# Optimization experiments

Hardware: AMD Instinct MI355X
Metric: run time of the kernel (lower is better)

The kernel has to match this reference:

```python
import jax, jax.numpy as jnp
import numpy as np

B, C, T, V = 8, 64, 16, 207
H, WSZ = 8, 4
EPS = 1e-5


def setup_inputs() -> dict:
    key = jax.random.key(0)
    ks = jax.random.split(key, 16)
    def w(k, shape):
        return jax.random.normal(k, shape, jnp.float32) * 0.02
    inp = {"x": jax.random.normal(ks[0], (B, C, T, V), jnp.float32)}
    for i, s in enumerate("ab"):
        o = 1 + i * 4
        inp[f"qkv_w_{s}"] = w(ks[o], (C, 3 * C))
        inp[f"qkv_b_{s}"] = jnp.zeros((3 * C,), jnp.float32)
        inp[f"proj_w_{s}"] = w(ks[o + 1], (C, C))
        inp[f"proj_b_{s}"] = jnp.zeros((C,), jnp.float32)
        inp[f"ffn_w1_{s}"] = w(ks[o + 2], (C, 4 * C))
        inp[f"ffn_b1_{s}"] = jnp.zeros((4 * C,), jnp.float32)
        inp[f"ffn_w2_{s}"] = w(ks[o + 3], (4 * C, C))
        inp[f"ffn_b2_{s}"] = jnp.zeros((C,), jnp.float32)
        inp[f"ln_{s}1_g"] = jnp.ones((C, T, V), jnp.float32)
        inp[f"ln_{s}1_b"] = jnp.zeros((C, T, V), jnp.float32)
        inp[f"ln_{s}2_g"] = jnp.ones((C, T, V), jnp.float32)
        inp[f"ln_{s}2_b"] = jnp.zeros((C, T, V), jnp.float32)
    inp["n_head"] = H
    inp["window_size"] = WSZ
    return inp


def _layer_norm(x, g, b):
    # LayerNorm over (C, T, V) dims of [B, C, T, V]
    mu = jnp.mean(x, axis=(1, 2, 3), keepdims=True)
    var = jnp.var(x, axis=(1, 2, 3), keepdims=True)
    return (x - mu) / jnp.sqrt(var + EPS) * g + b


def _window_att(x, wqkv, bqkv, wo, bo, n_head, wsz):
    # Joint spatio-temporal attention within windows of `wsz` timesteps.
    b_, c_, t_, v_ = x.shape
    nw = t_ // wsz
    dh = c_ // n_head
    # [B,C,T,V] -> [B,T,V,C] -> [B,nW, wsz*V, C]
    xt = jnp.transpose(x, (0, 2, 3, 1)).reshape(b_, nw, wsz * v_, c_)
    qkv = xt @ wqkv + bqkv  # [B,nW,N,3C]
    q, k, v = jnp.split(qkv, 3, axis=-1)
    def heads(t):
        return t.reshape(b_, nw, -1, n_head, dh).transpose(0, 1, 3, 2, 4)  # [B,nW,H,N,dh]
    q, k, v = heads(q), heads(k), heads(v)
    scale = 1.0 / jnp.sqrt(jnp.asarray(dh, jnp.float32))
    att = jax.nn.softmax(jnp.einsum('bwhnd,bwhmd->bwhnm', q, k) * scale, axis=-1)
    out = jnp.einsum('bwhnm,bwhmd->bwhnd', att, v)
    out = out.transpose(0, 1, 3, 2, 4).reshape(b_, nw, wsz * v_, c_) @ wo + bo
    return out.reshape(b_, t_, v_, c_).transpose(0, 3, 1, 2)


def _ffn(x, w1, b1, w2, b2):
    h = jax.nn.relu(jnp.einsum('bctv,cd->bdtv', x, w1) + b1[None, :, None, None])
    return jnp.einsum('bdtv,dc->bctv', h, w2) + b2[None, :, None, None]


def _block(x, wqkv, bqkv, wo, bo, w1, b1, w2, b2, g1, be1, g2, be2, n_head, wsz):
    x = _window_att(x, wqkv, bqkv, wo, bo, n_head, wsz) + x
    x = _layer_norm(x, g1, be1)
    x = _ffn(x, w1, b1, w2, b2) + x
    x = _layer_norm(x, g2, be2)
    # cyclic shift along time by shift_pixel = wsz // 2
    return jnp.roll(x, -(wsz // 2), axis=2)


def reference(x, qkv_w_a, qkv_b_a, proj_w_a, proj_b_a, ffn_w1_a, ffn_b1_a, ffn_w2_a, ffn_b2_a,
              ln_a1_g, ln_a1_b, ln_a2_g, ln_a2_b,
              qkv_w_b, qkv_b_b, proj_w_b, proj_b_b, ffn_w1_b, ffn_b1_b, ffn_w2_b, ffn_b2_b,
              ln_b1_g, ln_b1_b, ln_b2_g, ln_b2_b, n_head, window_size):
    x = _block(x, qkv_w_a, qkv_b_a, proj_w_a, proj_b_a, ffn_w1_a, ffn_b1_a, ffn_w2_a, ffn_b2_a,
               ln_a1_g, ln_a1_b, ln_a2_g, ln_a2_b, n_head, window_size)
    x = _block(x, qkv_w_b, qkv_b_b, proj_w_b, proj_b_b, ffn_w1_b, ffn_b1_b, ffn_w2_b, ffn_b2_b,
               ln_b1_g, ln_b1_b, ln_b2_g, ln_b2_b, n_head, window_size)
    return x
```

## Files before the change

kernel.cpp:

```cpp
#include <hip/hip_runtime.h>
#include <hip/hip_bf16.h>

#define Bb  8
#define Cc  64
#define Tt  16
#define Vv  207
#define Hh  8
#define DH  8
#define NW  4
#define WSZ 4
#define Nn  (WSZ*Vv)
#define NP  832
#define TV  (Tt*Vv)
#define CTV (Cc*Tt*Vv)
#define S   (Bb*CTV)
#define NBWH (Bb*NW*Hh)
#define EPSF 1e-5f
#define QSCALE 0.51006971401146f

typedef __attribute__((ext_vector_type(4))) short bf16x4;
typedef __attribute__((ext_vector_type(4))) float f32x4;
typedef __attribute__((ext_vector_type(2))) unsigned int u32x2;

static __device__ __forceinline__ short f2bf(float f) {
    union { float f; unsigned u; } v; v.f = f;
    unsigned r = (v.u + 0x7FFFu + ((v.u >> 16) & 1u)) >> 16;
    return (short)r;
}

static __device__ __forceinline__ bf16x4 pack4(float a, float b, float c, float d) {
    unsigned ua = __builtin_bit_cast(unsigned, a) + 0x8000u;
    unsigned ub = __builtin_bit_cast(unsigned, b) + 0x8000u;
    unsigned uc = __builtin_bit_cast(unsigned, c) + 0x8000u;
    unsigned ud = __builtin_bit_cast(unsigned, d) + 0x8000u;
    u32x2 t;
    t[0] = (ua >> 16) | (ub & 0xFFFF0000u);
    t[1] = (uc >> 16) | (ud & 0xFFFF0000u);
    return __builtin_bit_cast(bf16x4, t);
}

__global__ void prep_kernel(short* __restrict__ qb, short* __restrict__ kb,
                            short* __restrict__ vtb, float* __restrict__ stats) {
    int i = blockIdx.x*256 + threadIdx.x;
    if (i < 64) stats[i] = 0.f;
    if (i < NBWH*NP*8) {
        int bwh = i / (NP*8); int rest = i % (NP*8);
        int n = rest >> 3; int d = 8 + (rest & 7);
        kb[((size_t)bwh*NP + n)*16 + d] = 0;
        int d2 = 8 + rest / NP; int n2 = rest % NP;
        vtb[((size_t)bwh*16 + d2)*NP + n2] = (d2 == 8) ? (short)0x3F80 : (short)0;
    }
    if (i < NBWH*32) {
        int bwh = i >> 5; int rest = i & 31;
        int n = Nn + (rest >> 3); int d = rest & 7;
        qb[((size_t)bwh*NP + n)*8 + d] = 0;
        kb[((size_t)bwh*NP + n)*16 + d] = 0;
        int d3 = rest >> 2; int n3 = Nn + (rest & 3);
        vtb[((size_t)bwh*16 + d3)*NP + n3] = 0;
    }
}

__global__ __launch_bounds__(256) void qkv_kernel(const float* __restrict__ xin,
        const float* __restrict__ w, const float* __restrict__ bias,
        short* __restrict__ qb, short* __restrict__ kb, short* __restrict__ vtb) {
    __shared__ short wqs[3072*4];
    __shared__ float bqs[192];
    int tid = threadIdx.x;
    int b = blockIdx.x / 52;
    int r0 = (blockIdx.x % 52) * 64;
    const float* xb = xin + (size_t)b*CTV;
    for (int s = tid; s < 3072; s += 256) {
        int nt = s >> 8; int kc = (s >> 6) & 3; int ln = s & 63;
        int li = ln & 15; int q = ln >> 4;
        bf16x4 f;
        #pragma unroll
        for (int j = 0; j < 4; ++j)
            f[j] = f2bf(w[(kc*16 + q*4 + j)*192 + nt*16 + li]);
        *((bf16x4*)&wqs[s*4]) = f;
    }
    if (tid < 192) bqs[tid] = bias[tid];
    __syncthreads();

    int lane = tid & 63; int wv = tid >> 6;
    int l15 = lane & 15; int quad = lane >> 4;
    int r = r0 + wv*16 + l15;
    bool valid = r < TV;
    int rc = valid ? r : TV-1;
    bf16x4 xf[4];
    #pragma unroll
    for (int kc = 0; kc < 4; ++kc) {
        #pragma unroll
        for (int j = 0; j < 4; ++j)
            xf[kc][j] = f2bf(xb[(size_t)(kc*16 + quad*4 + j)*TV + rc]);
    }
    int t = rc / Vv; int vv = rc % Vv;
    int w_ = t >> 2; int tw = t & 3;
    int n = tw*Vv + vv;
    int bwbase = (b*NW + w_)*Hh;

    #pragma unroll
    for (int nt = 0; nt < 12; ++nt) {
        float4 bb = *((const float4*)&bqs[nt*16 + quad*4]);
        f32x4 acc = {bb.x, bb.y, bb.z, bb.w};
        #pragma unroll
        for (int kc = 0; kc < 4; ++kc) {
            bf16x4 wf = *((const bf16x4*)&wqs[((nt*4 + kc)*64 + lane)*4]);
            acc = __builtin_amdgcn_mfma_f32_16x16x16bf16_1k(wf, xf[kc], acc, 0, 0, 0);
        }
        if (valid) {
            int which = nt >> 2;
            #pragma unroll
            for (int j = 0; j < 4; ++j) {
                int cc = (nt & 3)*16 + quad*4 + j;
                int h = cc >> 3; int d = cc & 7;
                int bwh = bwbase + h;
                if (which == 0)      qb[((size_t)bwh*NP + n)*8 + d] = f2bf(acc[j]*QSCALE);
                else if (which == 1) kb[((size_t)bwh*NP + n)*16 + d] = f2bf(acc[j]);
                else                 vtb[((size_t)bwh*16 + d)*NP + n] = f2bf(acc[j]);
            }
        }
    }
}

__global__ __launch_bounds__(1024) void attn_kernel(const short* __restrict__ qb,
        const short* __restrict__ kb, const short* __restrict__ vtb,
        short* __restrict__ att) {
    __shared__ short ks[NP*20];
    __shared__ short vs[10*840];
    int bwh = blockIdx.x;
    int tid = threadIdx.x;
    int lane = tid & 63;
    int wv = tid >> 6;
    int quad = lane >> 4;
    int l15 = lane & 15;

    const u32x2* kg = (const u32x2*)(kb + (size_t)bwh*NP*16);
    for (int idx = tid; idx < NP*4; idx += 1024) {
        int n = idx >> 2; int j = idx & 3;
        *((u32x2*)&ks[n*20 + j*4]) = kg[idx];
    }
    const u32x2* vg = (const u32x2*)(vtb + (size_t)bwh*16*NP);
    for (int idx = tid; idx < 9*208; idx += 1024) {
        int rr = idx / 208; int j = idx % 208;
        *((u32x2*)&vs[rr*840 + j*4]) = vg[rr*208 + j];
    }
    if (tid < 210) *((u32x2*)&vs[9*840 + tid*4]) = (u32x2){0u, 0u};
    __syncthreads();

    int nm = (wv < 4) ? 4 : 3;
    const short* qbase = qb + (size_t)bwh*NP*8;
    bf16x4 aq[4];
    f32x4 oacc[4];
    #pragma unroll
    for (int i = 0; i < 4; ++i) {
        aq[i] = (bf16x4){0,0,0,0};
        oacc[i] = (f32x4){0.f,0.f,0.f,0.f};
        if (i < nm && quad < 2)
            aq[i] = *(const bf16x4*)(qbase + (((wv + 16*i)*16 + l15)*8 + quad*4));
    }
    const short* kls = &ks[l15*20 + quad*4];
    const short* vls = &vs[((l15 < 9) ? l15 : 9)*840 + quad*4];

    for (int nt = 0; nt < 52; ++nt) {
        bf16x4 ak = *(const bf16x4*)(kls + nt*320);
        bf16x4 av = *(const bf16x4*)(vls + nt*16);
        bool mask = (nt == 51) && (quad == 3);
        #pragma unroll
        for (int i = 0; i < 4; ++i) {
            if (i < nm) {
                f32x4 s = __builtin_amdgcn_mfma_f32_16x16x16bf16_1k(
                              ak, aq[i], (f32x4){0.f,0.f,0.f,0.f}, 0, 0, 0);
                bf16x4 pb = pack4(__builtin_amdgcn_exp2f(s[0]), __builtin_amdgcn_exp2f(s[1]),
                                  __builtin_amdgcn_exp2f(s[2]), __builtin_amdgcn_exp2f(s[3]));
                if (mask) pb = (bf16x4){0,0,0,0};
                oacc[i] = __builtin_amdgcn_mfma_f32_16x16x16bf16_1k(av, pb, oacc[i], 0, 0, 0);
            }
        }
    }
    int h = bwh & 7; int bw = bwh >> 3;
    #pragma unroll
    for (int i = 0; i < 4; ++i) {
        if (i < nm) {
            float ls = __shfl(oacc[i][0], 32 + l15, 64);
            float inv = 1.f / ls;
            int m = (wv + 16*i)*16 + l15;
            if (quad < 2 && m < Nn) {
                bf16x4 ov = pack4(oacc[i][0]*inv, oacc[i][1]*inv,
                                  oacc[i][2]*inv, oacc[i][3]*inv);
                *((bf16x4*)&att[((size_t)bw*Nn + m)*Cc + h*DH + quad*4]) = ov;
            }
        }
    }
}

__global__ __launch_bounds__(256) void proj_kernel(const short* __restrict__ att,
        const float* __restrict__ wo, const float* __restrict__ bo,
        const float* __restrict__ resid, float* __restrict__ out,
        float* __restrict__ stats) {
    __shared__ short wos[1024*4];
    __shared__ float bos[64];
    __shared__ float r1[256], r2[256];
    int tid = threadIdx.x;
    int b = blockIdx.x / 52;
    int r0 = (blockIdx.x % 52) * 64;
    const float* xb = resid + (size_t)b*CTV;
    for (int s = tid; s < 1024; s += 256) {
        int nt = s >> 8; int kc = (s >> 6) & 3; int ln = s & 63;
        int li = ln & 15; int q = ln >> 4;
        bf16x4 f;
        #pragma unroll
        for (int j = 0; j < 4; ++j)
            f[j] = f2bf(wo[(kc*16 + q*4 + j)*64 + nt*16 + li]);
        *((bf16x4*)&wos[s*4]) = f;
    }
    if (tid < 64) bos[tid] = bo[tid];
    __syncthreads();

    int lane = tid & 63; int wv = tid >> 6;
    int l15 = lane & 15; int quad = lane >> 4;
    int r = r0 + wv*16 + l15;
    bool valid = r < TV;
    int rc = valid ? r : TV-1;
    int t = rc / Vv; int vv = rc % Vv;
    int w_ = t >> 2; int tw = t & 3;
    int n = tw*Vv + vv;
    int bw = b*NW + w_;
    const short* arow = att + ((size_t)bw*Nn + n)*Cc;
    bf16x4 af[4];
    #pragma unroll
    for (int kc = 0; kc < 4; ++kc)
        af[kc] = *((const bf16x4*)&arow[kc*16 + quad*4]);

    f32x4 acc[4];
    #pragma unroll
    for (int nt = 0; nt < 4; ++nt) {
        float4 bb = *((const float4*)&bos[nt*16 + quad*4]);
        acc[nt] = (f32x4){bb.x, bb.y, bb.z, bb.w};
        #pragma unroll
        for (int kc = 0; kc < 4; ++kc) {
            bf16x4 wf = *((const bf16x4*)&wos[((nt*4 + kc)*64 + lane)*4]);
            acc[nt] = __builtin_amdgcn_mfma_f32_16x16x16bf16_1k(wf, af[kc], acc[nt], 0, 0, 0);
        }
    }
    float s1 = 0.f, s2 = 0.f;
    if (valid) {
        #pragma unroll
        for (int nt = 0; nt < 4; ++nt) {
            #pragma unroll
            for (int j = 0; j < 4; ++j) {
                int c_out = nt*16 + quad*4 + j;
                size_t oi = (size_t)b*CTV + (size_t)c_out*TV + r;
                float val = acc[nt][j] + xb[(size_t)c_out*TV + r];
                out[oi] = val;
                s1 += val; s2 += val*val;
            }
        }
    }
    r1[tid] = s1; r2[tid] = s2;
    __syncthreads();
    for (int o = 128; o > 0; o >>= 1) {
        if (tid < o) { r1[tid] += r1[tid+o]; r2[tid] += r2[tid+o]; }
        __syncthreads();
    }
    if (tid == 0) { atomicAdd(&stats[b*2], r1[0]); atomicAdd(&stats[b*2+1], r2[0]); }
}

__global__ void ln_apply_kernel(const float* __restrict__ x,
                                const float* __restrict__ g,
                                const float* __restrict__ be,
                                const float* __restrict__ stats,
                                float* __restrict__ out,
                                int shift) {
    int idx = blockIdx.x*256 + threadIdx.x;
    if (idx >= S) return;
    int b = idx / CTV; int r = idx % CTV;
    int c = r / TV; int q2 = r % TV; int t = q2 / Vv; int vv = q2 % Vv;
    float mean = stats[b*2] * (1.0f/CTV);
    float var  = stats[b*2+1] * (1.0f/CTV) - mean*mean;
    float rstd = rsqrtf(var + EPSF);
    float val = (x[idx]-mean)*rstd*g[r] + be[r];
    int tout = (t - shift + Tt) % Tt;
    size_t oidx = ((size_t)(b*Cc + c)*Tt + tout)*Vv + vv;
    out[oidx] = val;
}

__global__ __launch_bounds__(256) void ffn_kernel(const float* __restrict__ xin,
        const float* __restrict__ w1, const float* __restrict__ b1,
        const float* __restrict__ w2, const float* __restrict__ b2,
        float* __restrict__ out, float* __restrict__ stats) {
    __shared__ short w1s[4096*4];
    __shared__ short w2s[4096*4];
    __shared__ short xsf[1024*4];
    __shared__ float b1s[256];
    __shared__ float b2s[64];
    __shared__ float r1s[256], r2s[256];
    int tid = threadIdx.x;
    int b = blockIdx.x / 52;
    int r0 = (blockIdx.x % 52) * 64;
    const float* xb = xin + (size_t)b*CTV;

    for (int s2 = tid; s2 < 4096; s2 += 256) {
        int nt = s2 >> 8; int kc = (s2 >> 6) & 3; int ln = s2 & 63;
        int l15 = ln & 15; int quad = ln >> 4;
        bf16x4 f;
        #pragma unroll
        for (int j = 0; j < 4; ++j)
            f[j] = f2bf(w1[(kc*16 + quad*4 + j)*256 + nt*16 + l15]);
        *((bf16x4*)&w1s[s2*4]) = f;
    }
    for (int s2 = tid; s2 < 4096; s2 += 256) {
        int nt = s2 >> 8; int ct = (s2 >> 6) & 3; int ln = s2 & 63;
        int l15 = ln & 15; int quad = ln >> 4;
        bf16x4 f;
        #pragma unroll
        for (int j = 0; j < 4; ++j)
            f[j] = f2bf(w2[(nt*16 + quad*4 + j)*64 + ct*16 + l15]);
        *((bf16x4*)&w2s[s2*4]) = f;
    }
    for (int s2 = tid; s2 < 1024; s2 += 256) {
        int wv2 = s2 >> 8; int kc = (s2 >> 6) & 3; int ln = s2 & 63;
        int l15 = ln & 15; int quad = ln >> 4;
        int r = r0 + wv2*16 + l15; if (r >= TV) r = TV-1;
        bf16x4 f;
        #pragma unroll
        for (int j = 0; j < 4; ++j)
            f[j] = f2bf(xb[(size_t)(kc*16 + quad*4 + j)*TV + r]);
        *((bf16x4*)&xsf[s2*4]) = f;
    }
    b1s[tid] = b1[tid];
    if (tid < 64) b2s[tid] = b2[tid];
    __syncthreads();

    int lane = tid & 63; int wv = tid >> 6;
    int l15 = lane & 15; int quad = lane >> 4;
    bf16x4 xf[4];
    #pragma unroll
    for (int kc = 0; kc < 4; ++kc)
        xf[kc] = *((const bf16x4*)&xsf[((wv*4 + kc)*64 + lane)*4]);

    f32x4 oacc[4];
    #pragma unroll
    for (int ct = 0; ct < 4; ++ct) oacc[ct] = (f32x4){0.f,0.f,0.f,0.f};

    for (int nt = 0; nt < 16; ++nt) {
        float4 bb = *((const float4*)&b1s[nt*16 + quad*4]);
        f32x4 acc = {bb.x, bb.y, bb.z, bb.w};
        #pragma unroll
        for (int kc = 0; kc < 4; ++kc) {
            bf16x4 wf = *((const bf16x4*)&w1s[((nt*4 + kc)*64 + lane)*4]);
            acc = __builtin_amdgcn_mfma_f32_16x16x16bf16_1k(wf, xf[kc], acc, 0, 0, 0);
        }
        bf16x4 pf = pack4(fmaxf(acc[0], 0.f), fmaxf(acc[1], 0.f),
                          fmaxf(acc[2], 0.f), fmaxf(acc[3], 0.f));
        #pragma unroll
        for (int ct = 0; ct < 4; ++ct) {
            bf16x4 wf2 = *((const bf16x4*)&w2s[((nt*4 + ct)*64 + lane)*4]);
            oacc[ct] = __builtin_amdgcn_mfma_f32_16x16x16bf16_1k(wf2, pf, oacc[ct], 0, 0, 0);
        }
    }
    int r = r0 + wv*16 + l15;
    float s1 = 0.f, s2 = 0.f;
    if (r < TV) {
        #pragma unroll
        for (int ct = 0; ct < 4; ++ct) {
            #pragma unroll
            for (int j = 0; j < 4; ++j) {
                int c_out = ct*16 + quad*4 + j;
                size_t oi = (size_t)b*CTV + (size_t)c_out*TV + r;
                float val = oacc[ct][j] + b2s[c_out] + xb[(size_t)c_out*TV + r];
                out[oi] = val;
                s1 += val; s2 += val*val;
            }
        }
    }
    r1s[tid] = s1; r2s[tid] = s2;
    __syncthreads();
    for (int o = 128; o > 0; o >>= 1) {
        if (tid < o) { r1s[tid] += r1s[tid+o]; r2s[tid] += r2s[tid+o]; }
        __syncthreads();
    }
    if (tid == 0) { atomicAdd(&stats[b*2], r1s[0]); atomicAdd(&stats[b*2+1], r2s[0]); }
}

extern "C" void kernel_launch(void* const* d_in, const int* in_sizes, int n_in,
                              void* d_out, int out_size, void* d_ws, size_t ws_size,
                              hipStream_t stream) {
    const float* xin = (const float*)d_in[0];

    float* bufA  = (float*)d_ws;
    float* bufB  = bufA + S;
    float* stats = bufB + S;
    short* qb    = (short*)(stats + 64);
    short* kb    = qb + (size_t)NBWH*NP*8;
    short* vtb   = kb + (size_t)NBWH*NP*16;
    short* att   = vtb + (size_t)NBWH*16*NP;

    prep_kernel<<<(NBWH*NP*8 + 255)/256, 256, 0, stream>>>(qb, kb, vtb, stats);

    for (int blk = 0; blk < 2; ++blk) {
        int o = 1 + blk*12;
        const float* qkvw = (const float*)d_in[o+0];
        const float* qkvb = (const float*)d_in[o+1];
        const float* pw   = (const float*)d_in[o+2];
        const float* pb   = (const float*)d_in[o+3];
        const float* fw1  = (const float*)d_in[o+4];
        const float* fb1  = (const float*)d_in[o+5];
        const float* fw2  = (const float*)d_in[o+6];
        const float* fb2  = (const float*)d_in[o+7];
        const float* g1   = (const float*)d_in[o+8];
        const float* be1  = (const float*)d_in[o+9];
        const float* g2   = (const float*)d_in[o+10];
        const float* be2  = (const float*)d_in[o+11];
        float* st1 = stats + blk*32;
        float* st2 = st1 + 16;

        const float* src = (blk == 0) ? xin : bufA;

        qkv_kernel<<<Bb*52, 256, 0, stream>>>(src, qkvw, qkvb, qb, kb, vtb);
        attn_kernel<<<NBWH, 1024, 0, stream>>>(qb, kb, vtb, att);
        proj_kernel<<<Bb*52, 256, 0, stream>>>(att, pw, pb, src, bufB, st1);
        ln_apply_kernel<<<S/256, 256, 0, stream>>>(bufB, g1, be1, st1, bufA, 0);
        ffn_kernel<<<Bb*52, 256, 0, stream>>>(bufA, fw1, fb1, fw2, fb2, bufB, st2);
        bool fin = (blk == 1);
        ln_apply_kernel<<<S/256, 256, 0, stream>>>(bufB, g2, be2, st2,
                                                   fin ? (float*)d_out : bufA,
                                                   WSZ/2);
    }
}
```

Baseline: 306.0 us.

## Fuse layer-norm apply and time roll into consumer GEMM kernels

Removes three of the four standalone layer-norm apply passes. Normalisation, with the cyclic time shift done through index remapping, now runs inside the loads of the qkv, proj and ffn kernels. The qkv kernel also stages its outputs in shared memory so it can write q, k and v with wider, more contiguous stores. This saves full-tensor read/write round trips and kernel launches, at the cost of recomputing the normalisation at each consumer and reading gamma/beta there. The ffn kernel now writes its output in place over its input buffer, which depends on each block touching only its own rows.

```diff
diff --git a/kernel.cpp b/kernel.cpp
--- a/kernel.cpp
+++ b/kernel.cpp
@@ -60,15 +60,17 @@
     }
 }
 
-__global__ __launch_bounds__(256) void qkv_kernel(const float* __restrict__ xin,
+__global__ __launch_bounds__(256) void qkv_kernel(const float* __restrict__ src,
+        const float* __restrict__ st, const float* __restrict__ g, const float* __restrict__ be,
         const float* __restrict__ w, const float* __restrict__ bias,
         short* __restrict__ qb, short* __restrict__ kb, short* __restrict__ vtb) {
     __shared__ short wqs[3072*4];
     __shared__ float bqs[192];
+    __shared__ short os[64*196];
     int tid = threadIdx.x;
     int b = blockIdx.x / 52;
     int r0 = (blockIdx.x % 52) * 64;
-    const float* xb = xin + (size_t)b*CTV;
+    const float* xb = src + (size_t)b*CTV;
     for (int s = tid; s < 3072; s += 256) {
         int nt = s >> 8; int kc = (s >> 6) & 3; int ln = s & 63;
         int li = ln & 15; int q = ln >> 4;
@@ -84,20 +86,29 @@
     int lane = tid & 63; int wv = tid >> 6;
     int l15 = lane & 15; int quad = lane >> 4;
     int r = r0 + wv*16 + l15;
-    bool valid = r < TV;
-    int rc = valid ? r : TV-1;
+    int rc = (r < TV) ? r : TV-1;
+    int t = rc / Vv; int vv = rc - t*Vv;
+    float mean = 0.f, rstd = 0.f; int off;
+    if (st) {
+        mean = st[b*2] * (1.0f/CTV);
+        float var = st[b*2+1] * (1.0f/CTV) - mean*mean;
+        rstd = rsqrtf(var + EPSF);
+        off = ((t+2)&15)*Vv + vv;
+    } else off = rc;
+
     bf16x4 xf[4];
     #pragma unroll
     for (int kc = 0; kc < 4; ++kc) {
         #pragma unroll
-        for (int j = 0; j < 4; ++j)
-            xf[kc][j] = f2bf(xb[(size_t)(kc*16 + quad*4 + j)*TV + rc]);
-    }
-    int t = rc / Vv; int vv = rc % Vv;
-    int w_ = t >> 2; int tw = t & 3;
-    int n = tw*Vv + vv;
-    int bwbase = (b*NW + w_)*Hh;
-
+        for (int j = 0; j < 4; ++j) {
+            int idx = (kc*16 + quad*4 + j)*TV + off;
+            float xv = xb[idx];
+            if (st) xv = (xv - mean)*rstd*g[idx] + be[idx];
+            xf[kc][j] = f2bf(xv);
+        }
+    }
+
+    f32x4 accv[12];
     #pragma unroll
     for (int nt = 0; nt < 12; ++nt) {
         float4 bb = *((const float4*)&bqs[nt*16 + quad*4]);
@@ -107,18 +118,45 @@
             bf16x4 wf = *((const bf16x4*)&wqs[((nt*4 + kc)*64 + lane)*4]);
             acc = __builtin_amdgcn_mfma_f32_16x16x16bf16_1k(wf, xf[kc], acc, 0, 0, 0);
         }
-        if (valid) {
-            int which = nt >> 2;
-            #pragma unroll
-            for (int j = 0; j < 4; ++j) {
-                int cc = (nt & 3)*16 + quad*4 + j;
-                int h = cc >> 3; int d = cc & 7;
-                int bwh = bwbase + h;
-                if (which == 0)      qb[((size_t)bwh*NP + n)*8 + d] = f2bf(acc[j]*QSCALE);
-                else if (which == 1) kb[((size_t)bwh*NP + n)*16 + d] = f2bf(acc[j]);
-                else                 vtb[((size_t)bwh*16 + d)*NP + n] = f2bf(acc[j]);
-            }
-        }
+        accv[nt] = acc;
+    }
+
+    int pos = wv*16 + l15;
+    #pragma unroll
+    for (int nt = 0; nt < 12; ++nt) {
+        f32x4 a = accv[nt];
+        bf16x4 pk = (nt < 4) ? pack4(a[0]*QSCALE, a[1]*QSCALE, a[2]*QSCALE, a[3]*QSCALE)
+                             : pack4(a[0], a[1], a[2], a[3]);
+        *((bf16x4*)&os[pos*196 + nt*16 + quad*4]) = pk;
+    }
+    __syncthreads();
+
+    int pp = tid & 63;
+    int rr = r0 + pp;
+    bool pv = rr < TV;
+    int rrc = pv ? rr : TV-1;
+    int t4 = rrc / Vv; int vv4 = rrc - t4*Vv;
+    int n2 = (t4 & 3)*Vv + vv4;
+    int wbase = (b*NW + (t4 >> 2))*Hh;
+    #pragma unroll
+    for (int i = 0; i < 2; ++i) {
+        int h = i*4 + wv;
+        if (pv) {
+            bf16x4 q0 = *((const bf16x4*)&os[pp*196 + h*8]);
+            bf16x4 q1 = *((const bf16x4*)&os[pp*196 + h*8 + 4]);
+            short* qd = &qb[((size_t)(wbase + h)*NP + n2)*8];
+            *((bf16x4*)qd) = q0; *((bf16x4*)(qd+4)) = q1;
+            bf16x4 k0 = *((const bf16x4*)&os[pp*196 + 64 + h*8]);
+            bf16x4 k1 = *((const bf16x4*)&os[pp*196 + 64 + h*8 + 4]);
+            short* kd = &kb[((size_t)(wbase + h)*NP + n2)*16];
+            *((bf16x4*)kd) = k0; *((bf16x4*)(kd+4)) = k1;
+        }
+    }
+    #pragma unroll
+    for (int i = 0; i < 16; ++i) {
+        int hd = i*4 + wv;
+        if (pv)
+            vtb[((size_t)(wbase + (hd >> 3))*16 + (hd & 7))*NP + n2] = os[pp*196 + 128 + hd];
     }
 }
 
@@ -195,8 +233,9 @@
 
 __global__ __launch_bounds__(256) void proj_kernel(const short* __restrict__ att,
         const float* __restrict__ wo, const float* __restrict__ bo,
-        const float* __restrict__ resid, float* __restrict__ out,
-        float* __restrict__ stats) {
+        const float* __restrict__ resid,
+        const float* __restrict__ st, const float* __restrict__ g, const float* __restrict__ be,
+        float* __restrict__ out, float* __restrict__ stats) {
     __shared__ short wos[1024*4];
     __shared__ float bos[64];
     __shared__ float r1[256], r2[256];
@@ -221,10 +260,9 @@
     int r = r0 + wv*16 + l15;
     bool valid = r < TV;
     int rc = valid ? r : TV-1;
-    int t = rc / Vv; int vv = rc % Vv;
-    int w_ = t >> 2; int tw = t & 3;
-    int n = tw*Vv + vv;
-    int bw = b*NW + w_;
+    int t = rc / Vv; int vv = rc - t*Vv;
+    int n = (t & 3)*Vv + vv;
+    int bw = b*NW + (t >> 2);
     const short* arow = att + ((size_t)bw*Nn + n)*Cc;
     bf16x4 af[4];
     #pragma unroll
@@ -242,6 +280,13 @@
             acc[nt] = __builtin_amdgcn_mfma_f32_16x16x16bf16_1k(wf, af[kc], acc[nt], 0, 0, 0);
         }
     }
+    float mean = 0.f, rstd = 0.f; int off;
+    if (st) {
+        mean = st[b*2] * (1.0f/CTV);
+        float var = st[b*2+1] * (1.0f/CTV) - mean*mean;
+        rstd = rsqrtf(var + EPSF);
+        off = ((t+2)&15)*Vv + vv;
+    } else off = rc;
     float s1 = 0.f, s2 = 0.f;
     if (valid) {
         #pragma unroll
@@ -249,9 +294,11 @@
             #pragma unroll
             for (int j = 0; j < 4; ++j) {
                 int c_out = nt*16 + quad*4 + j;
-                size_t oi = (size_t)b*CTV + (size_t)c_out*TV + r;
-                float val = acc[nt][j] + xb[(size_t)c_out*TV + r];
-                out[oi] = val;
+                int ridx = c_out*TV + off;
+                float xv = xb[ridx];
+                if (st) xv = (xv - mean)*rstd*g[ridx] + be[ridx];
+                float val = acc[nt][j] + xv;
+                out[(size_t)b*CTV + (size_t)c_out*TV + r] = val;
                 s1 += val; s2 += val*val;
             }
         }
@@ -285,6 +332,7 @@
 }
 
 __global__ __launch_bounds__(256) void ffn_kernel(const float* __restrict__ xin,
+        const float* __restrict__ st, const float* __restrict__ g, const float* __restrict__ be,
         const float* __restrict__ w1, const float* __restrict__ b1,
         const float* __restrict__ w2, const float* __restrict__ b2,
         float* __restrict__ out, float* __restrict__ stats) {
@@ -298,6 +346,9 @@
     int b = blockIdx.x / 52;
     int r0 = (blockIdx.x % 52) * 64;
     const float* xb = xin + (size_t)b*CTV;
+    float mean = st[b*2] * (1.0f/CTV);
+    float var  = st[b*2+1] * (1.0f/CTV) - mean*mean;
+    float rstd = rsqrtf(var + EPSF);
 
     for (int s2 = tid; s2 < 4096; s2 += 256) {
         int nt = s2 >> 8; int kc = (s2 >> 6) & 3; int ln = s2 & 63;
@@ -323,8 +374,10 @@
         int r = r0 + wv2*16 + l15; if (r >= TV) r = TV-1;
         bf16x4 f;
         #pragma unroll
-        for (int j = 0; j < 4; ++j)
-            f[j] = f2bf(xb[(size_t)(kc*16 + quad*4 + j)*TV + r]);
+        for (int j = 0; j < 4; ++j) {
+            int idx = (kc*16 + quad*4 + j)*TV + r;
+            f[j] = f2bf((xb[idx] - mean)*rstd*g[idx] + be[idx]);
+        }
         *((bf16x4*)&xsf[s2*4]) = f;
     }
     b1s[tid] = b1[tid];
@@ -366,9 +419,10 @@
             #pragma unroll
             for (int j = 0; j < 4; ++j) {
                 int c_out = ct*16 + quad*4 + j;
-                size_t oi = (size_t)b*CTV + (size_t)c_out*TV + r;
-                float val = oacc[ct][j] + b2s[c_out] + xb[(size_t)c_out*TV + r];
-                out[oi] = val;
+                int idx = c_out*TV + r;
+                float xv = (xb[idx] - mean)*rstd*g[idx] + be[idx];
+                float val = oacc[ct][j] + b2s[c_out] + xv;
+                out[(size_t)b*CTV + idx] = val;
                 s1 += val; s2 += val*val;
             }
         }
@@ -395,35 +449,45 @@
     short* vtb   = kb + (size_t)NBWH*NP*16;
     short* att   = vtb + (size_t)NBWH*16*NP;
 
+    const float* A0  = (const float*)d_in[1+0*12];
+    const float* A1  = (const float*)d_in[1+0*12+1];
+    const float* A2  = (const float*)d_in[1+0*12+2];
+    const float* A3  = (const float*)d_in[1+0*12+3];
+    const float* A4  = (const float*)d_in[1+0*12+4];
+    const float* A5  = (const float*)d_in[1+0*12+5];
+    const float* A6  = (const float*)d_in[1+0*12+6];
+    const float* A7  = (const float*)d_in[1+0*12+7];
+    const float* A8  = (const float*)d_in[1+0*12+8];
+    const float* A9  = (const float*)d_in[1+0*12+9];
+    const float* A10 = (const float*)d_in[1+0*12+10];
+    const float* A11 = (const float*)d_in[1+0*12+11];
+    const float* B0  = (const float*)d_in[1+1*12];
+    const float* B1  = (const float*)d_in[1+1*12+1];
+    const float* B2  = (const float*)d_in[1+1*12+2];
+    const float* B3  = (const float*)d_in[1+1*12+3];
+    const float* B4  = (const float*)d_in[1+1*12+4];
+    const float* B5  = (const float*)d_in[1+1*12+5];
+    const float* B6  = (const float*)d_in[1+1*12+6];
+    const float* B7  = (const float*)d_in[1+1*12+7];
+    const float* B8  = (const float*)d_in[1+1*12+8];
+    const float* B9  = (const float*)d_in[1+1*12+9];
+    const float* B10 = (const float*)d_in[1+1*12+10];
+    const float* B11 = (const float*)d_in[1+1*12+11];
+
+    float* st1a = stats + 0;
+    float* st2a = stats + 16;
+    float* st1b = stats + 32;
+    float* st2b = stats + 48;
+
     prep_kernel<<<(NBWH*NP*8 + 255)/256, 256, 0, stream>>>(qb, kb, vtb, stats);
 
-    for (int blk = 0; blk < 2; ++blk) {
-        int o = 1 + blk*12;
-        const float* qkvw = (const float*)d_in[o+0];
-        const float* qkvb = (const float*)d_in[o+1];
-        const float* pw   = (const float*)d_in[o+2];
-        const float* pb   = (const float*)d_in[o+3];
-        const float* fw1  = (const float*)d_in[o+4];
-        const float* fb1  = (const float*)d_in[o+5];
-        const float* fw2  = (const float*)d_in[o+6];
-        const float* fb2  = (const float*)d_in[o+7];
-        const float* g1   = (const float*)d_in[o+8];
-        const float* be1  = (const float*)d_in[o+9];
-        const float* g2   = (const float*)d_in[o+10];
-        const float* be2  = (const float*)d_in[o+11];
-        float* st1 = stats + blk*32;
-        float* st2 = st1 + 16;
-
-        const float* src = (blk == 0) ? xin : bufA;
-
-        qkv_kernel<<<Bb*52, 256, 0, stream>>>(src, qkvw, qkvb, qb, kb, vtb);
-        attn_kernel<<<NBWH, 1024, 0, stream>>>(qb, kb, vtb, att);
-        proj_kernel<<<Bb*52, 256, 0, stream>>>(att, pw, pb, src, bufB, st1);
-        ln_apply_kernel<<<S/256, 256, 0, stream>>>(bufB, g1, be1, st1, bufA, 0);
-        ffn_kernel<<<Bb*52, 256, 0, stream>>>(bufA, fw1, fb1, fw2, fb2, bufB, st2);
-        bool fin = (blk == 1);
-        ln_apply_kernel<<<S/256, 256, 0, stream>>>(bufB, g2, be2, st2,
-                                                   fin ? (float*)d_out : bufA,
-                                                   WSZ/2);
-    }
-}
+    qkv_kernel<<<Bb*52, 256, 0, stream>>>(xin, nullptr, nullptr, nullptr, A0, A1, qb, kb, vtb);
+    attn_kernel<<<NBWH, 1024, 0, stream>>>(qb, kb, vtb, att);
+    proj_kernel<<<Bb*52, 256, 0, stream>>>(att, A2, A3, xin, nullptr, nullptr, nullptr, bufB, st1a);
+    ffn_kernel<<<Bb*52, 256, 0, stream>>>(bufB, st1a, A8, A9, A4, A5, A6, A7, bufB, st2a);
+    qkv_kernel<<<Bb*52, 256, 0, stream>>>(bufB, st2a, A10, A11, B0, B1, qb, kb, vtb);
+    attn_kernel<<<NBWH, 1024, 0, stream>>>(qb, kb, vtb, att);
+    proj_kernel<<<Bb*52, 256, 0, stream>>>(att, B2, B3, bufB, st2a, A10, A11, bufA, st1b);
+    ffn_kernel<<<Bb*52, 256, 0, stream>>>(bufA, st1b, B8, B9, B4, B5, B6, B7, bufA, st2b);
+    ln_apply_kernel<<<(S+255)/256, 256, 0, stream>>>(bufA, B10, B11, st2b, (float*)d_out, WSZ/2);
+}
```

New measurement: 304.3 us. Within noise of the previous version (-0.6%).
